# Kernel tuning notes

Hardware: AMD Instinct MI355X
Metric: run time of the kernel (lower is better)

Reference implementation:

```python
import jax, jax.numpy as jnp
import numpy as np

CHANNELS = 128
M_MODES = 64
B = 128
N = 4096


def setup_inputs() -> dict:
    key = jax.random.key(0)
    k1, k2, k3 = jax.random.split(key, 3)
    h = jax.random.normal(k1, (B * N, CHANNELS), dtype=jnp.float32)
    U = jax.random.normal(k2, (B, N, M_MODES), dtype=jnp.float32)
    W = jax.random.normal(k3, (M_MODES, CHANNELS, CHANNELS), dtype=jnp.float32) * 0.02
    ptr = jnp.arange(B + 1, dtype=jnp.int64) * N  # equal-size segments
    return {"h": h, "U": U, "W": W, "ptr": ptr}


def reference(h, U, W, ptr):
    # U: [B, N, m]; h: [B*N, C]; W: [m, C, C]
    b, n, m = U.shape
    hb = h.reshape(b, n, -1)                              # [B, N, C]
    h_hat = jnp.einsum('bnm,bnc->bmc', U, hb)             # U^T h per graph
    out_hat = jnp.einsum('bmc,mco->bmo', h_hat, W)        # per-mode channel mix
    out = jnp.einsum('bnm,bmo->bno', U, out_hat)          # back to node space
    return out.reshape(h.shape)
```

## Files before the change

### kernel.cpp

```cpp
#include <hip/hip_runtime.h>

#define CH 128
#define MM 64
#define BB 128
#define NN 4096
#define KSPLIT 8
#define KCHUNK (NN / KSPLIT)
#define KU 8
#define NIT (KCHUNK / KU)

#define AS1(p) ((const __attribute__((address_space(1))) void*)(p))
#define AS3(p) ((__attribute__((address_space(3))) void*)(p))

typedef __bf16 bf16x8 __attribute__((ext_vector_type(8)));
typedef float  f32x4  __attribute__((ext_vector_type(4)));

__device__ __forceinline__ void gl_lds16(const float* g, float* l) {
    __builtin_amdgcn_global_load_lds(AS1(g), AS3(l), 16, 0, 0);
}

__global__ __launch_bounds__(128) void k1_uth(const float* __restrict__ U,
                                              const float* __restrict__ h,
                                              float* __restrict__ hhp) {
    __shared__ float panel[2][1536];

    const int tid = threadIdx.x;
    const int bid = blockIdx.x;
    const int b   = bid >> 3;
    const int ks  = bid & 7;
    const int k0  = ks * KCHUNK;

    const int mt = tid >> 4;
    const int ct = tid & 15;

    const float* Ub = U + ((size_t)b * NN + k0) * MM;
    const float* hb = h + ((size_t)b * NN + k0) * CH;

    float acc[8][8];
    #pragma unroll
    for (int i = 0; i < 8; ++i)
        #pragma unroll
        for (int j = 0; j < 8; ++j) acc[i][j] = 0.f;

    auto stage = [&](int p, int it) {
        const float* us = Ub + (size_t)it * KU * MM;
        const float* hs = hb + (size_t)it * KU * CH;
        gl_lds16(us + tid * 4,       &panel[p][tid * 4]);
        gl_lds16(hs + tid * 4,       &panel[p][512 + tid * 4]);
        gl_lds16(hs + 512 + tid * 4, &panel[p][1024 + tid * 4]);
    };

    auto compute = [&](const float* __restrict__ P) {
        #pragma unroll
        for (int ku = 0; ku < KU; ++ku) {
            float4 u0 = *(const float4*)&P[ku * 64 + mt * 8];
            float4 u1 = *(const float4*)&P[ku * 64 + mt * 8 + 4];
            float4 h0 = *(const float4*)&P[512 + ku * 128 + ct * 4];
            float4 h1 = *(const float4*)&P[512 + ku * 128 + 64 + ct * 4];
            float u[8]  = {u0.x, u0.y, u0.z, u0.w, u1.x, u1.y, u1.z, u1.w};
            float hv[8] = {h0.x, h0.y, h0.z, h0.w, h1.x, h1.y, h1.z, h1.w};
            #pragma unroll
            for (int i = 0; i < 8; ++i)
                #pragma unroll
                for (int j = 0; j < 8; ++j)
                    acc[i][j] += u[i] * hv[j];
        }
    };

    stage(0, 0);
    #pragma unroll 1
    for (int it = 0; it < NIT - 1; ++it) {
        stage((it + 1) & 1, it + 1);
        asm volatile("s_waitcnt vmcnt(3)" ::: "memory");
        __builtin_amdgcn_s_barrier();
        __builtin_amdgcn_sched_barrier(0);
        compute(panel[it & 1]);
        __builtin_amdgcn_s_barrier();
    }
    asm volatile("s_waitcnt vmcnt(0)" ::: "memory");
    __builtin_amdgcn_s_barrier();
    __builtin_amdgcn_sched_barrier(0);
    compute(panel[(NIT - 1) & 1]);

    float* dst = hhp + ((size_t)(b * KSPLIT + ks) * MM + mt * 8) * CH;
    #pragma unroll
    for (int i = 0; i < 8; ++i) {
        *(float4*)&dst[i * CH + ct * 4] =
            make_float4(acc[i][0], acc[i][1], acc[i][2], acc[i][3]);
        *(float4*)&dst[i * CH + 64 + ct * 4] =
            make_float4(acc[i][4], acc[i][5], acc[i][6], acc[i][7]);
    }
}

__global__ __launch_bounds__(256) void k2_mix(const float* __restrict__ hhp,
                                              const float* __restrict__ W,
                                              __bf16* __restrict__ ohf) {
    __shared__ float hs[16][CH];
    const int tid  = threadIdx.x;
    const int o    = tid & 127;
    const int half = tid >> 7;
    const int m    = blockIdx.x;
    const int b0   = blockIdx.y * 16;

    #pragma unroll
    for (int i = 0; i < 8; ++i) {
        const int b = b0 + half * 8 + i;
        const float* src = hhp + ((size_t)(b * KSPLIT) * MM + m) * CH + o;
        float s = 0.f;
        #pragma unroll
        for (int ksi = 0; ksi < KSPLIT; ++ksi)
            s += src[(size_t)ksi * MM * CH];
        hs[half * 8 + i][o] = s;
    }
    __syncthreads();

    float acc[8];
    #pragma unroll
    for (int i = 0; i < 8; ++i) acc[i] = 0.f;

    const float* Wm = W + (size_t)m * CH * CH;
    for (int c = 0; c < CH; ++c) {
        const float w = Wm[c * CH + o];
        #pragma unroll
        for (int i = 0; i < 8; ++i) acc[i] += hs[half * 8 + i][c] * w;
    }

    const int mt      = m >> 5;
    const int m5      = m & 31;
    const int lane_hi = m5 >> 3;
    const int j       = m5 & 7;
    const int ot      = o >> 4;
    const int lane    = lane_hi * 16 + (o & 15);
    const size_t eidx = ((size_t)(mt * 8 + ot) * 64 + lane) * 8 + j;

    #pragma unroll
    for (int i = 0; i < 8; ++i) {
        const int b = b0 + half * 8 + i;
        ohf[(size_t)b * 8192 + eidx] = (__bf16)acc[i];
    }
}

__global__ __launch_bounds__(256) void k3_back(const float* __restrict__ U,
                                               const __bf16* __restrict__ ohf,
                                               float* __restrict__ out) {
    const int tid  = threadIdx.x;
    const int lane = tid & 63;
    const int wv   = tid >> 6;
    const int n0   = blockIdx.x * 64;
    const int b    = blockIdx.y;

    const bf16x8* ohfb = (const bf16x8*)(ohf + (size_t)b * 8192);
    bf16x8 bf[2][8];
    #pragma unroll
    for (int mt = 0; mt < 2; ++mt)
        #pragma unroll
        for (int ot = 0; ot < 8; ++ot)
            bf[mt][ot] = ohfb[(mt * 8 + ot) * 64 + lane];

    const float* arow = U + ((size_t)b * NN + n0 + wv * 16 + (lane & 15)) * MM
                          + ((lane >> 4) << 3);
    bf16x8 af[2];
    #pragma unroll
    for (int mt = 0; mt < 2; ++mt) {
        float4 a0 = *(const float4*)(arow + mt * 32);
        float4 a1 = *(const float4*)(arow + mt * 32 + 4);
        af[mt][0] = (__bf16)a0.x; af[mt][1] = (__bf16)a0.y;
        af[mt][2] = (__bf16)a0.z; af[mt][3] = (__bf16)a0.w;
        af[mt][4] = (__bf16)a1.x; af[mt][5] = (__bf16)a1.y;
        af[mt][6] = (__bf16)a1.z; af[mt][7] = (__bf16)a1.w;
    }

    f32x4 acc[8];
    #pragma unroll
    for (int ot = 0; ot < 8; ++ot) acc[ot] = (f32x4){0.f, 0.f, 0.f, 0.f};

    #pragma unroll
    for (int ot = 0; ot < 8; ++ot) {
        acc[ot] = __builtin_amdgcn_mfma_f32_16x16x32_bf16(af[0], bf[0][ot], acc[ot], 0, 0, 0);
        acc[ot] = __builtin_amdgcn_mfma_f32_16x16x32_bf16(af[1], bf[1][ot], acc[ot], 0, 0, 0);
    }

    float* dst = out + ((size_t)b * NN + n0 + wv * 16 + (lane >> 4) * 4) * CH + (lane & 15);
    #pragma unroll
    for (int ot = 0; ot < 8; ++ot)
        #pragma unroll
        for (int r = 0; r < 4; ++r)
            dst[(size_t)r * CH + ot * 16] = acc[ot][r];
}

extern "C" void kernel_launch(void* const* d_in, const int* in_sizes, int n_in,
                              void* d_out, int out_size, void* d_ws, size_t ws_size,
                              hipStream_t stream) {
    const float* h = (const float*)d_in[0];
    const float* U = (const float*)d_in[1];
    const float* W = (const float*)d_in[2];
    float* out = (float*)d_out;

    float*  hhp = (float*)d_out;
    __bf16* ohf = (__bf16*)d_ws;

    k1_uth<<<BB * KSPLIT, 128, 0, stream>>>(U, h, hhp);
    k2_mix<<<dim3(MM, BB / 16), 256, 0, stream>>>(hhp, W, ohf);
    k3_back<<<dim3(NN / 64, BB), 256, 0, stream>>>(U, ohf, out);
}
```

Baseline: 239.9 us.

## Rewrite U^T h reduction kernel with bf16 MFMA and register double-buffering

The first-stage U^T h kernel drops its fp32 FMA outer-product over LDS panels filled by global_load_lds. It now converts U and h tiles to bf16 in registers and accumulates with 16x16x32 MFMA, using a register double buffer with no LDS. The K split drops from 8 to 4 and the block grows to 256 threads with four waves. This cuts FP32 ALU cost and the LDS traffic, but the loads are strided scalar reads rather than vectorized ones, and bf16 inputs lose precision in the reduction.

```diff
diff --git a/kernel.cpp b/kernel.cpp
--- a/kernel.cpp
+++ b/kernel.cpp
@@ -4,92 +4,92 @@
 #define MM 64
 #define BB 128
 #define NN 4096
-#define KSPLIT 8
+#define KSPLIT 4
 #define KCHUNK (NN / KSPLIT)
-#define KU 8
-#define NIT (KCHUNK / KU)
-
-#define AS1(p) ((const __attribute__((address_space(1))) void*)(p))
-#define AS3(p) ((__attribute__((address_space(3))) void*)(p))
+#define NSTEP (KCHUNK / 32)
 
 typedef __bf16 bf16x8 __attribute__((ext_vector_type(8)));
 typedef float  f32x4  __attribute__((ext_vector_type(4)));
 
-__device__ __forceinline__ void gl_lds16(const float* g, float* l) {
-    __builtin_amdgcn_global_load_lds(AS1(g), AS3(l), 16, 0, 0);
-}
-
-__global__ __launch_bounds__(128) void k1_uth(const float* __restrict__ U,
-                                              const float* __restrict__ h,
-                                              float* __restrict__ hhp) {
-    __shared__ float panel[2][1536];
-
-    const int tid = threadIdx.x;
-    const int bid = blockIdx.x;
-    const int b   = bid >> 3;
-    const int ks  = bid & 7;
-    const int k0  = ks * KCHUNK;
-
-    const int mt = tid >> 4;
-    const int ct = tid & 15;
-
-    const float* Ub = U + ((size_t)b * NN + k0) * MM;
-    const float* hb = h + ((size_t)b * NN + k0) * CH;
-
-    float acc[8][8];
-    #pragma unroll
-    for (int i = 0; i < 8; ++i)
-        #pragma unroll
-        for (int j = 0; j < 8; ++j) acc[i][j] = 0.f;
-
-    auto stage = [&](int p, int it) {
-        const float* us = Ub + (size_t)it * KU * MM;
-        const float* hs = hb + (size_t)it * KU * CH;
-        gl_lds16(us + tid * 4,       &panel[p][tid * 4]);
-        gl_lds16(hs + tid * 4,       &panel[p][512 + tid * 4]);
-        gl_lds16(hs + 512 + tid * 4, &panel[p][1024 + tid * 4]);
+__global__ __launch_bounds__(256, 2) void k1_uth(const float* __restrict__ U,
+                                                 const float* __restrict__ h,
+                                                 float* __restrict__ hhp) {
+    const int tid  = threadIdx.x;
+    const int lane = tid & 63;
+    const int wv   = tid >> 6;
+    const int b    = blockIdx.x >> 2;
+    const int ks   = blockIdx.x & 3;
+    const int k0   = ks * KCHUNK;
+
+    const int l15 = lane & 15;
+    const int lk  = (lane >> 4) * 8;
+
+    const float* Ua = U + ((size_t)b * NN + k0 + lk) * MM + l15;
+    const float* ha = h + ((size_t)b * NN + k0 + lk) * CH + wv * 32 + l15;
+
+    float ar[2][4][8];
+    float br[2][2][8];
+
+    auto load_step = [&](int buf, int step) {
+        const float* ua = Ua + (size_t)step * 32 * MM;
+        const float* hb = ha + (size_t)step * 32 * CH;
+        #pragma unroll
+        for (int mt = 0; mt < 4; ++mt)
+            #pragma unroll
+            for (int j = 0; j < 8; ++j)
+                ar[buf][mt][j] = ua[j * MM + mt * 16];
+        #pragma unroll
+        for (int ci = 0; ci < 2; ++ci)
+            #pragma unroll
+            for (int j = 0; j < 8; ++j)
+                br[buf][ci][j] = hb[j * CH + ci * 16];
     };
 
-    auto compute = [&](const float* __restrict__ P) {
-        #pragma unroll
-        for (int ku = 0; ku < KU; ++ku) {
-            float4 u0 = *(const float4*)&P[ku * 64 + mt * 8];
-            float4 u1 = *(const float4*)&P[ku * 64 + mt * 8 + 4];
-            float4 h0 = *(const float4*)&P[512 + ku * 128 + ct * 4];
-            float4 h1 = *(const float4*)&P[512 + ku * 128 + 64 + ct * 4];
-            float u[8]  = {u0.x, u0.y, u0.z, u0.w, u1.x, u1.y, u1.z, u1.w};
-            float hv[8] = {h0.x, h0.y, h0.z, h0.w, h1.x, h1.y, h1.z, h1.w};
-            #pragma unroll
-            for (int i = 0; i < 8; ++i)
-                #pragma unroll
-                for (int j = 0; j < 8; ++j)
-                    acc[i][j] += u[i] * hv[j];
-        }
+    f32x4 acc[4][2];
+    #pragma unroll
+    for (int mt = 0; mt < 4; ++mt)
+        #pragma unroll
+        for (int ci = 0; ci < 2; ++ci)
+            acc[mt][ci] = (f32x4){0.f, 0.f, 0.f, 0.f};
+
+    auto compute = [&](int buf) {
+        bf16x8 af[4], bfr[2];
+        #pragma unroll
+        for (int mt = 0; mt < 4; ++mt)
+            #pragma unroll
+            for (int j = 0; j < 8; ++j)
+                af[mt][j] = (__bf16)ar[buf][mt][j];
+        #pragma unroll
+        for (int ci = 0; ci < 2; ++ci)
+            #pragma unroll
+            for (int j = 0; j < 8; ++j)
+                bfr[ci][j] = (__bf16)br[buf][ci][j];
+        #pragma unroll
+        for (int mt = 0; mt < 4; ++mt)
+            #pragma unroll
+            for (int ci = 0; ci < 2; ++ci)
+                acc[mt][ci] = __builtin_amdgcn_mfma_f32_16x16x32_bf16(
+                    af[mt], bfr[ci], acc[mt][ci], 0, 0, 0);
     };
 
-    stage(0, 0);
-    #pragma unroll 1
-    for (int it = 0; it < NIT - 1; ++it) {
-        stage((it + 1) & 1, it + 1);
-        asm volatile("s_waitcnt vmcnt(3)" ::: "memory");
-        __builtin_amdgcn_s_barrier();
-        __builtin_amdgcn_sched_barrier(0);
-        compute(panel[it & 1]);
-        __builtin_amdgcn_s_barrier();
-    }
-    asm volatile("s_waitcnt vmcnt(0)" ::: "memory");
-    __builtin_amdgcn_s_barrier();
-    __builtin_amdgcn_sched_barrier(0);
-    compute(panel[(NIT - 1) & 1]);
-
-    float* dst = hhp + ((size_t)(b * KSPLIT + ks) * MM + mt * 8) * CH;
-    #pragma unroll
-    for (int i = 0; i < 8; ++i) {
-        *(float4*)&dst[i * CH + ct * 4] =
-            make_float4(acc[i][0], acc[i][1], acc[i][2], acc[i][3]);
-        *(float4*)&dst[i * CH + 64 + ct * 4] =
-            make_float4(acc[i][4], acc[i][5], acc[i][6], acc[i][7]);
-    }
+    load_step(0, 0);
+    #pragma unroll 2
+    for (int t = 0; t < NSTEP - 1; ++t) {
+        load_step((t + 1) & 1, t + 1);
+        compute(t & 1);
+    }
+    compute((NSTEP - 1) & 1);
+
+    float* dst = hhp + (size_t)(b * KSPLIT + ks) * MM * CH;
+    const int rowbase = (lane >> 4) * 4;
+    #pragma unroll
+    for (int mt = 0; mt < 4; ++mt)
+        #pragma unroll
+        for (int ci = 0; ci < 2; ++ci)
+            #pragma unroll
+            for (int r = 0; r < 4; ++r)
+                dst[(size_t)(mt * 16 + rowbase + r) * CH + wv * 32 + ci * 16 + l15] =
+                    acc[mt][ci][r];
 }
 
 __global__ __launch_bounds__(256) void k2_mix(const float* __restrict__ hhp,
@@ -199,7 +199,7 @@
     float*  hhp = (float*)d_out;
     __bf16* ohf = (__bf16*)d_ws;
 
-    k1_uth<<<BB * KSPLIT, 128, 0, stream>>>(U, h, hhp);
+    k1_uth<<<BB * KSPLIT, 256, 0, stream>>>(U, h, hhp);
     k2_mix<<<dim3(MM, BB / 16), 256, 0, stream>>>(hhp, W, ohf);
     k3_back<<<dim3(NN / 64, BB), 256, 0, stream>>>(U, ohf, out);
 }
```

Result: faster. 220.9 us (-7.9%).
